# Optimization experiments

Measured on AMD Instinct MI355X. Metric: run time of the kernel, lower is better.

Reference implementation:

```python
import jax, jax.numpy as jnp
import numpy as np

NUM_CLASSES = 3
NUM_YAW = 2
BOX_DOF = 7
C_IN = 384


def setup_inputs() -> dict:
    key = jax.random.key(0)
    k1, k2, k3 = jax.random.split(key, 3)
    B, ny, nx = 4, 200, 176
    feature_map = jax.random.normal(k1, (B, C_IN, ny, nx), dtype=jnp.float32)
    # conv weights: 1x1 convs -> plain matrices [C_out, C_in]
    Wc = 0.01 * jax.random.normal(k2, (NUM_CLASSES * NUM_YAW, C_IN), dtype=jnp.float32)
    # bias init: constant_(-log(1-0.01)/0.01) per module _init_weights
    bc = jnp.full((NUM_CLASSES * NUM_YAW,), -np.log(1.0 - 0.01) / 0.01, dtype=jnp.float32)
    Wr = 0.01 * jax.random.normal(k3, (NUM_CLASSES * NUM_YAW * BOX_DOF, C_IN), dtype=jnp.float32)
    br = jnp.zeros((NUM_CLASSES * NUM_YAW * BOX_DOF,), dtype=jnp.float32)
    return {"feature_map": feature_map, "Wc": Wc, "bc": bc, "Wr": Wr, "br": br}


def reference(feature_map, Wc, bc, Wr, br):
    B, _, ny, nx = feature_map.shape
    # 1x1 conv == channel GEMM
    cls_raw = jnp.einsum('bchw,oc->bohw', feature_map, Wc) + bc[None, :, None, None]
    reg_raw = jnp.einsum('bchw,oc->bohw', feature_map, Wr) + br[None, :, None, None]
    # reshape_cls: (B, NUM_CLASSES, NUM_YAW, ny, nx)
    cls_map = cls_raw.reshape(B, NUM_CLASSES, NUM_YAW, ny, nx)
    # reshape_reg: view (B, n_cls, DOF, NUM_YAW, ny, nx) then permute(0,1,3,4,5,2)
    reg_map = reg_raw.reshape(B, NUM_CLASSES, BOX_DOF, NUM_YAW, ny, nx)
    reg_map = jnp.transpose(reg_map, (0, 1, 3, 4, 5, 2))  # (B, n_cls, yaw, ny, nx, DOF)
    return (cls_map, reg_map)
```

## Files before the change

kernel.cpp:

```cpp
#include <hip/hip_runtime.h>


#define C_IN   384
#define N_CLS  6
#define N_REG  42
#define N_OUT  48
#define NY     200
#define NX     176
#define NPIX   (NY * NX)
#define NBATCH 4
#define CLS_ELEMS (NBATCH * N_CLS * NPIX)
#define TOTAL_PIX (NBATCH * NPIX)

__global__ __launch_bounds__(256) void prep_weights(
    const float* __restrict__ Wc, const float* __restrict__ bc,
    const float* __restrict__ Wr, const float* __restrict__ br,
    float* __restrict__ Wt, float* __restrict__ bias) {
  int idx = blockIdx.x * 256 + threadIdx.x;
  if (idx < C_IN * N_OUT) {
    int k = idx / N_OUT;
    int o = idx - k * N_OUT;
    Wt[idx] = (o < N_CLS) ? Wc[o * C_IN + k] : Wr[(o - N_CLS) * C_IN + k];
  }
  if (idx < N_OUT) bias[idx] = (idx < N_CLS) ? bc[idx] : br[idx - N_CLS];
}

__global__ __launch_bounds__(256, 2) void proposal_main(
    const float* __restrict__ feat, const float* __restrict__ Wt,
    const float* __restrict__ bias, float* __restrict__ out) {
  const int pix = blockIdx.x * 256 + threadIdx.x;
  const int b = pix / NPIX;
  const int p = pix - b * NPIX;
  const float* __restrict__ f = feat + b * (C_IN * NPIX) + p;

  float acc[N_OUT];
#pragma unroll
  for (int o = 0; o < N_OUT; ++o) acc[o] = bias[o];

  constexpr int U = 8;
  float vbuf[U];
#pragma unroll
  for (int u = 0; u < U; ++u) vbuf[u] = f[u * NPIX];

  for (int k0 = 0; k0 < C_IN - U; k0 += U) {
    float vnext[U];
#pragma unroll
    for (int u = 0; u < U; ++u) vnext[u] = f[(k0 + U + u) * NPIX];
#pragma unroll
    for (int u = 0; u < U; ++u) {
      const float* __restrict__ w = Wt + (k0 + u) * N_OUT;
#pragma unroll
      for (int o = 0; o < N_OUT; ++o) acc[o] = fmaf(vbuf[u], w[o], acc[o]);
    }
#pragma unroll
    for (int u = 0; u < U; ++u) vbuf[u] = vnext[u];
  }
  {
    const int k0 = C_IN - U;
#pragma unroll
    for (int u = 0; u < U; ++u) {
      const float* __restrict__ w = Wt + (k0 + u) * N_OUT;
#pragma unroll
      for (int o = 0; o < N_OUT; ++o) acc[o] = fmaf(vbuf[u], w[o], acc[o]);
    }
  }

  float* __restrict__ out_cls = out;
  float* __restrict__ out_reg = out + CLS_ELEMS;
#pragma unroll
  for (int o = 0; o < N_CLS; ++o)
    out_cls[(b * N_CLS + o) * NPIX + p] = acc[o];
#pragma unroll
  for (int r = 0; r < N_REG; ++r) {
    const int c = r / 14;
    const int d = (r - c * 14) >> 1;
    const int y = r & 1;
    out_reg[((b * 3 + c) * 2 + y) * (NPIX * 7) + p * 7 + d] = acc[N_CLS + r];
  }
}

extern "C" void kernel_launch(void* const* d_in, const int* in_sizes, int n_in,
                              void* d_out, int out_size, void* d_ws, size_t ws_size,
                              hipStream_t stream) {
  const float* feat = (const float*)d_in[0];
  const float* Wc   = (const float*)d_in[1];
  const float* bc   = (const float*)d_in[2];
  const float* Wr   = (const float*)d_in[3];
  const float* br   = (const float*)d_in[4];
  float* outp = (float*)d_out;

  float* Wt   = (float*)d_ws;
  float* bias = Wt + C_IN * N_OUT;

  hipLaunchKernelGGL(prep_weights, dim3((C_IN * N_OUT + 255) / 256), dim3(256), 0, stream,
                     Wc, bc, Wr, br, Wt, bias);
  hipLaunchKernelGGL(proposal_main, dim3(TOTAL_PIX / 256), dim3(256), 0, stream,
                     feat, Wt, bias, outp);
}
```

Baseline: 348.5 us.

## Replace scalar FMA channel GEMM with bf16 MFMA using LDS-staged weight fragments

Rewrites the 1x1-conv GEMM to use 16x16x32 bf16 MFMA instructions. Weights are pre-packed into per-lane fragment layout and copied into LDS once per block. Feature values are converted to bf16 on the fly, with a one-step register prefetch of the next 32 channels. This cuts the VALU work of the FP32 scalar loop. In exchange, the bf16 rounding of both inputs and weights loosens accuracy, and the feature-map read, which is likely the dominant memory traffic, is unchanged.

```diff
diff --git a/kernel.cpp b/kernel.cpp
--- a/kernel.cpp
+++ b/kernel.cpp
@@ -2,81 +2,111 @@
 
 
 #define C_IN   384
-#define N_CLS  6
-#define N_REG  42
+#define NPIX   35200
+#define NBATCH 4
 #define N_OUT  48
-#define NY     200
-#define NX     176
-#define NPIX   (NY * NX)
-#define NBATCH 4
-#define CLS_ELEMS (NBATCH * N_CLS * NPIX)
-#define TOTAL_PIX (NBATCH * NPIX)
+#define KSTEPS 12
+#define WFRAG_ELEMS (KSTEPS * 3 * 64 * 8)
+#define CLS_ELEMS (NBATCH * 6 * NPIX)
+
+typedef __attribute__((ext_vector_type(8))) short bf16x8;
+typedef __attribute__((ext_vector_type(4))) float f32x4;
+
+static __device__ __forceinline__ short f2bf(float f) {
+  union { float f; unsigned u; } v; v.f = f;
+  unsigned r = v.u + 0x7FFFu + ((v.u >> 16) & 1u);
+  return (short)(r >> 16);
+}
 
 __global__ __launch_bounds__(256) void prep_weights(
     const float* __restrict__ Wc, const float* __restrict__ bc,
     const float* __restrict__ Wr, const float* __restrict__ br,
-    float* __restrict__ Wt, float* __restrict__ bias) {
+    short* __restrict__ Wfrag, float* __restrict__ bias) {
   int idx = blockIdx.x * 256 + threadIdx.x;
-  if (idx < C_IN * N_OUT) {
-    int k = idx / N_OUT;
-    int o = idx - k * N_OUT;
-    Wt[idx] = (o < N_CLS) ? Wc[o * C_IN + k] : Wr[(o - N_CLS) * C_IN + k];
+  if (idx < WFRAG_ELEMS) {
+    int j = idx & 7;
+    int l = (idx >> 3) & 63;
+    int t = (idx >> 9) % 3;
+    int s = idx / 1536;
+    int o = t * 16 + (l & 15);
+    int k = s * 32 + 8 * (l >> 4) + j;
+    float w = (o < 6) ? Wc[o * C_IN + k] : Wr[(o - 6) * C_IN + k];
+    Wfrag[idx] = f2bf(w);
   }
-  if (idx < N_OUT) bias[idx] = (idx < N_CLS) ? bc[idx] : br[idx - N_CLS];
+  if (idx < N_OUT) bias[idx] = (idx < 6) ? bc[idx] : br[idx - 6];
 }
 
-__global__ __launch_bounds__(256, 2) void proposal_main(
-    const float* __restrict__ feat, const float* __restrict__ Wt,
+__global__ __launch_bounds__(512) void proposal_mfma(
+    const float* __restrict__ feat, const short* __restrict__ Wfrag,
     const float* __restrict__ bias, float* __restrict__ out) {
-  const int pix = blockIdx.x * 256 + threadIdx.x;
-  const int b = pix / NPIX;
-  const int p = pix - b * NPIX;
-  const float* __restrict__ f = feat + b * (C_IN * NPIX) + p;
+  __shared__ short wlds[WFRAG_ELEMS];
 
-  float acc[N_OUT];
+  {
+    const f32x4* __restrict__ src = (const f32x4*)Wfrag;
+    f32x4* dst = (f32x4*)wlds;
+    for (int i = threadIdx.x; i < WFRAG_ELEMS / 8; i += 512) dst[i] = src[i];
+  }
+
+  const int lane = threadIdx.x & 63;
+  const int wave = threadIdx.x >> 6;
+  const int g  = lane >> 4;
+  const int lc = lane & 15;
+  const int gp = blockIdx.x * 128 + wave * 16;
+  const int b  = gp / NPIX;
+  const int p  = gp - b * NPIX;
+
+  const float* __restrict__ fbase =
+      feat + (size_t)(b * C_IN + 8 * g) * NPIX + p + lc;
+
+  f32x4 acc[3];
 #pragma unroll
-  for (int o = 0; o < N_OUT; ++o) acc[o] = bias[o];
+  for (int t = 0; t < 3; ++t)
+#pragma unroll
+    for (int r = 0; r < 4; ++r) acc[t][r] = bias[t * 16 + 4 * g + r];
 
-  constexpr int U = 8;
-  float vbuf[U];
+  __syncthreads();
+
+  float fc[8], fn[8];
 #pragma unroll
-  for (int u = 0; u < U; ++u) vbuf[u] = f[u * NPIX];
+  for (int j = 0; j < 8; ++j) fc[j] = fbase[(size_t)j * NPIX];
 
-  for (int k0 = 0; k0 < C_IN - U; k0 += U) {
-    float vnext[U];
+  for (int s = 0; s < KSTEPS; ++s) {
+    if (s + 1 < KSTEPS) {
 #pragma unroll
-    for (int u = 0; u < U; ++u) vnext[u] = f[(k0 + U + u) * NPIX];
+      for (int j = 0; j < 8; ++j)
+        fn[j] = fbase[(size_t)((s + 1) * 32 + j) * NPIX];
+    }
+    bf16x8 bf;
 #pragma unroll
-    for (int u = 0; u < U; ++u) {
-      const float* __restrict__ w = Wt + (k0 + u) * N_OUT;
+    for (int j = 0; j < 8; ++j) bf[j] = f2bf(fc[j]);
 #pragma unroll
-      for (int o = 0; o < N_OUT; ++o) acc[o] = fmaf(vbuf[u], w[o], acc[o]);
+    for (int t = 0; t < 3; ++t) {
+      bf16x8 af = *(const bf16x8*)(wlds + ((size_t)(s * 3 + t) * 64 + lane) * 8);
+      acc[t] = __builtin_amdgcn_mfma_f32_16x16x32_bf16(af, bf, acc[t], 0, 0, 0);
     }
 #pragma unroll
-    for (int u = 0; u < U; ++u) vbuf[u] = vnext[u];
-  }
-  {
-    const int k0 = C_IN - U;
-#pragma unroll
-    for (int u = 0; u < U; ++u) {
-      const float* __restrict__ w = Wt + (k0 + u) * N_OUT;
-#pragma unroll
-      for (int o = 0; o < N_OUT; ++o) acc[o] = fmaf(vbuf[u], w[o], acc[o]);
-    }
+    for (int j = 0; j < 8; ++j) fc[j] = fn[j];
   }
 
-  float* __restrict__ out_cls = out;
-  float* __restrict__ out_reg = out + CLS_ELEMS;
+  const int pp = p + lc;
 #pragma unroll
-  for (int o = 0; o < N_CLS; ++o)
-    out_cls[(b * N_CLS + o) * NPIX + p] = acc[o];
+  for (int t = 0; t < 3; ++t)
 #pragma unroll
-  for (int r = 0; r < N_REG; ++r) {
-    const int c = r / 14;
-    const int d = (r - c * 14) >> 1;
-    const int y = r & 1;
-    out_reg[((b * 3 + c) * 2 + y) * (NPIX * 7) + p * 7 + d] = acc[N_CLS + r];
-  }
+    for (int r = 0; r < 4; ++r) {
+      const int o = t * 16 + 4 * g + r;
+      const float v = acc[t][r];
+      if (o < 6) {
+        out[(size_t)(b * 6 + o) * NPIX + pp] = v;
+      } else {
+        const int q = o - 6;
+        const int c = q / 14;
+        const int qq = q - c * 14;
+        const int d = qq >> 1;
+        const int y = qq & 1;
+        out[CLS_ELEMS + (size_t)((b * 3 + c) * 2 + y) * (NPIX * 7)
+            + (size_t)pp * 7 + d] = v;
+      }
+    }
 }
 
 extern "C" void kernel_launch(void* const* d_in, const int* in_sizes, int n_in,
@@ -89,11 +119,11 @@
   const float* br   = (const float*)d_in[4];
   float* outp = (float*)d_out;
 
-  float* Wt   = (float*)d_ws;
-  float* bias = Wt + C_IN * N_OUT;
+  short* Wfrag = (short*)d_ws;
+  float* bias  = (float*)((char*)d_ws + WFRAG_ELEMS * sizeof(short));
 
-  hipLaunchKernelGGL(prep_weights, dim3((C_IN * N_OUT + 255) / 256), dim3(256), 0, stream,
-                     Wc, bc, Wr, br, Wt, bias);
-  hipLaunchKernelGGL(proposal_main, dim3(TOTAL_PIX / 256), dim3(256), 0, stream,
-                     feat, Wt, bias, outp);
+  hipLaunchKernelGGL(prep_weights, dim3((WFRAG_ELEMS + 255) / 256), dim3(256),
+                     0, stream, Wc, bc, Wr, br, Wfrag, bias);
+  hipLaunchKernelGGL(proposal_mfma, dim3(140800 / 128), dim3(512), 0, stream,
+                     feat, Wfrag, bias, outp);
 }
```

Result: faster. 317.5 us (-8.9%).
